# Kernel optimization log

Measured on AMD Instinct MI355X. Metric: run time of the kernel, lower is better.

## Reference

```python
import jax, jax.numpy as jnp
import numpy as np

N_NODES = 100000
N_EDGES = 1600000
D_IN = 128
D_OUT = 128


def setup_inputs() -> dict:
    key = jax.random.key(0)
    k1, k2, k3 = jax.random.split(key, 3)
    x = jax.random.normal(k1, (N_NODES, D_IN), dtype=jnp.float32)
    edge_indices = jax.random.randint(k2, (2, N_EDGES), 0, N_NODES, dtype=jnp.int64)
    # nn.Linear(input_dim, output_dim, bias=False): weight shape [out, in]
    W = jax.random.normal(k3, (D_OUT, D_IN), dtype=jnp.float32) * (1.0 / np.sqrt(D_IN))
    return {"x": x, "edge_indices": edge_indices, "W": W}


def reference(x, edge_indices, W):
    N = x.shape[0]
    # add self loops (i, i) for every node, as in create_norm_adj_mat
    self_loops = jnp.arange(N, dtype=edge_indices.dtype)
    row = jnp.concatenate([edge_indices[0], self_loops])  # [E+N]
    col = jnp.concatenate([edge_indices[1], self_loops])  # [E+N]
    # degree from row indices (torch.bincount(edge_indices[0]))
    deg = jax.ops.segment_sum(jnp.ones_like(row, dtype=x.dtype), row, num_segments=N)
    deg_rsqrt = jax.lax.rsqrt(deg)  # every node has a self loop -> deg >= 1
    vals = deg_rsqrt[row] * deg_rsqrt[col]  # [E+N] edge weights
    # dense linear projection first (linear(x)), then sparse aggregation
    h = x @ W.T  # [N, D_OUT]
    # (norm_adj_mat @ h)[i] = sum over edges with row==i of vals * h[col]
    agg = jax.ops.segment_sum(vals[:, None] * h[col], row, num_segments=N)  # [N, D_OUT]
    return jax.nn.relu(agg)
```

## Files before the change

### kernel.cpp

```cpp
#include <hip/hip_runtime.h>
#include <hip/hip_bf16.h>

#define D 128
#define SH 8
#define BROWS 256
#define NBK_MAX 512
#define CH 8192
#define CT 8
#define KS 4

typedef __bf16   bf16x8 __attribute__((ext_vector_type(8)));
typedef float    f32x4  __attribute__((ext_vector_type(4)));
typedef _Float16 f16x2  __attribute__((ext_vector_type(2)));
typedef _Float16 f16x4  __attribute__((ext_vector_type(4)));

__global__ __launch_bounds__(256) void k_zero(int* __restrict__ p, int n) {
    for (int i = blockIdx.x * blockDim.x + threadIdx.x; i < n; i += gridDim.x * blockDim.x)
        p[i] = 0;
}

__global__ __launch_bounds__(256) void k_bucket_count(const int* __restrict__ rows,
                                                      int* __restrict__ bcnt, int E, int NBK) {
    __shared__ int h[NBK_MAX];
    for (int i = threadIdx.x; i < NBK; i += 256) h[i] = 0;
    __syncthreads();
    for (int e = blockIdx.x * blockDim.x + threadIdx.x; e < E; e += gridDim.x * blockDim.x)
        atomicAdd(&h[rows[e] >> SH], 1);
    __syncthreads();
    for (int i = threadIdx.x; i < NBK; i += 256) {
        int v = h[i];
        if (v) atomicAdd(&bcnt[i], v);
    }
}

__global__ __launch_bounds__(512) void k_scan_buckets(const int* __restrict__ bcnt,
                                                      int* __restrict__ boff,
                                                      int* __restrict__ bcur,
                                                      int* __restrict__ row_start,
                                                      int NBK, int N, int E) {
    __shared__ int sd[512];
    int t = threadIdx.x;
    int own = (t < NBK) ? bcnt[t] : 0;
    sd[t] = own;
    __syncthreads();
    for (int off = 1; off < 512; off <<= 1) {
        int add = (t >= off) ? sd[t - off] : 0;
        __syncthreads();
        sd[t] += add;
        __syncthreads();
    }
    if (t < NBK) {
        int ex = sd[t] - own;
        boff[t] = ex;
        bcur[t] = ex;
    }
    if (t == 0) {
        boff[NBK] = E;
        row_start[N] = E;
    }
}

__global__ __launch_bounds__(256) void k_pairs(const int* __restrict__ rows,
                                               const int* __restrict__ cols,
                                               int* __restrict__ bcur,
                                               unsigned* __restrict__ pairs, int E, int NBK) {
    __shared__ int h[NBK_MAX];
    int e0 = blockIdx.x * CH;
    if (e0 >= E) return;
    int e1 = min(E, e0 + CH);
    for (int i = threadIdx.x; i < NBK; i += 256) h[i] = 0;
    __syncthreads();
    for (int e = e0 + threadIdx.x; e < e1; e += 256)
        atomicAdd(&h[rows[e] >> SH], 1);
    __syncthreads();
    for (int b = threadIdx.x; b < NBK; b += 256) {
        int v = h[b];
        h[b] = v ? atomicAdd(&bcur[b], v) : 0;
    }
    __syncthreads();
    for (int e = e0 + threadIdx.x; e < e1; e += 256) {
        int r = rows[e];
        int b = r >> SH;
        int p = atomicAdd(&h[b], 1);
        pairs[p] = ((unsigned)(r & (BROWS - 1)) << 24) | (unsigned)cols[e];
    }
}

__global__ __launch_bounds__(256) void k_bucket_finish(const unsigned* __restrict__ pairs,
                                                       const int* __restrict__ boff,
                                                       int* __restrict__ row_start,
                                                       float* __restrict__ dr,
                                                       int* __restrict__ csr_col, int N) {
    __shared__ int h[BROWS];
    __shared__ int cur[BROWS];
    int b = blockIdx.x;
    int t = threadIdx.x;
    int lim = min(N - (b << SH), BROWS);
    h[t] = 0;
    __syncthreads();
    int p0 = boff[b], p1 = boff[b + 1];
    for (int p = p0 + t; p < p1; p += 256)
        atomicAdd(&h[pairs[p] >> 24], 1);
    __syncthreads();
    int own = h[t];
    cur[t] = own;
    __syncthreads();
    for (int off = 1; off < 256; off <<= 1) {
        int add = (t >= off) ? cur[t - off] : 0;
        __syncthreads();
        cur[t] += add;
        __syncthreads();
    }
    int rs = p0 + cur[t] - own;
    if (t < lim) {
        row_start[(b << SH) + t] = rs;
        dr[(b << SH) + t] = rsqrtf((float)(own + 1));
    }
    __syncthreads();
    cur[t] = rs;
    __syncthreads();
    for (int p = p0 + t; p < p1; p += 256) {
        unsigned v = pairs[p];
        int rl = v >> 24;
        int q = atomicAdd(&cur[rl], 1);
        csr_col[q] = (int)(v & 0xFFFFFF);
    }
}

__global__ __launch_bounds__(256) void k_half_s(const float4* __restrict__ x4,
                                                const float* __restrict__ dr,
                                                f16x4* __restrict__ xh4, int n4) {
    for (int i = blockIdx.x * blockDim.x + threadIdx.x; i < n4; i += gridDim.x * blockDim.x) {
        float d = dr[i >> 5];
        float4 v = x4[i];
        xh4[i] = (f16x4){(_Float16)(v.x * d), (_Float16)(v.y * d),
                         (_Float16)(v.z * d), (_Float16)(v.w * d)};
    }
}

__global__ __launch_bounds__(256) void k_gather_s(const int* __restrict__ row_start,
                                                  const int* __restrict__ csr_col,
                                                  const _Float16* __restrict__ xh,
                                                  const float* __restrict__ dr,
                                                  float* __restrict__ out, int N) {
    int lane = threadIdx.x & 63;
    int gw = (blockIdx.x * blockDim.x + threadIdx.x) >> 6;
    int nw = (gridDim.x * blockDim.x) >> 6;
    for (int r = gw; r < N; r += nw) {
        float drr = dr[r];
        int beg = row_start[r], end = row_start[r + 1];
        const f16x2 xs = *(const f16x2*)&xh[(size_t)r * D + lane * 2];
        float a0 = (float)xs[0], a1 = (float)xs[1];
        for (int cb = beg; cb < end; cb += 64) {
            int m = end - cb;
            if (m > 64) m = 64;
            int cidx = (lane < m) ? csr_col[cb + lane] : 0;
            int j = 0;
            for (; j + 8 <= m; j += 8) {
                int c0 = __shfl(cidx, j);
                int c1 = __shfl(cidx, j + 1);
                int c2 = __shfl(cidx, j + 2);
                int c3 = __shfl(cidx, j + 3);
                int c4 = __shfl(cidx, j + 4);
                int c5 = __shfl(cidx, j + 5);
                int c6 = __shfl(cidx, j + 6);
                int c7 = __shfl(cidx, j + 7);
                f16x2 p0 = *(const f16x2*)&xh[(size_t)c0 * D + lane * 2];
                f16x2 p1 = *(const f16x2*)&xh[(size_t)c1 * D + lane * 2];
                f16x2 p2 = *(const f16x2*)&xh[(size_t)c2 * D + lane * 2];
                f16x2 p3 = *(const f16x2*)&xh[(size_t)c3 * D + lane * 2];
                f16x2 p4 = *(const f16x2*)&xh[(size_t)c4 * D + lane * 2];
                f16x2 p5 = *(const f16x2*)&xh[(size_t)c5 * D + lane * 2];
                f16x2 p6 = *(const f16x2*)&xh[(size_t)c6 * D + lane * 2];
                f16x2 p7 = *(const f16x2*)&xh[(size_t)c7 * D + lane * 2];
                a0 += (float)p0[0] + (float)p1[0] + (float)p2[0] + (float)p3[0]
                    + (float)p4[0] + (float)p5[0] + (float)p6[0] + (float)p7[0];
                a1 += (float)p0[1] + (float)p1[1] + (float)p2[1] + (float)p3[1]
                    + (float)p4[1] + (float)p5[1] + (float)p6[1] + (float)p7[1];
            }
            for (; j < m; ++j) {
                int c = __shfl(cidx, j);
                f16x2 p = *(const f16x2*)&xh[(size_t)c * D + lane * 2];
                a0 += (float)p[0];
                a1 += (float)p[1];
            }
        }
        float2 o;
        o.x = drr * a0;
        o.y = drr * a1;
        *(float2*)&out[(size_t)r * D + lane * 2] = o;
    }
}

__global__ __launch_bounds__(256) void k_project_mfma(const float* __restrict__ W,
                                                      float* __restrict__ out, int N) {
    __shared__ bf16x8 Bhi[CT * KS * 64];
    __shared__ bf16x8 Blo[CT * KS * 64];
    for (int f = threadIdx.x; f < CT * KS * 64; f += 256) {
        int l  = f & 63;
        int ks = (f >> 6) & 3;
        int ct = f >> 8;
        int o  = ct * 16 + (l & 15);
        int k0 = ks * 32 + ((l >> 4) * 8);
        const float* src = &W[o * D + k0];
        bf16x8 hi, lo;
#pragma unroll
        for (int i = 0; i < 8; ++i) {
            float v  = src[i];
            __bf16 h = (__bf16)v;
            hi[i] = h;
            lo[i] = (__bf16)(v - (float)h);
        }
        Bhi[f] = hi;
        Blo[f] = lo;
    }
    __syncthreads();

    int lane = threadIdx.x & 63;
    int wib  = threadIdx.x >> 6;
    int gw   = blockIdx.x * 4 + wib;
    int nw   = gridDim.x * 4;
    int nt   = N >> 4;
    int arow  = lane & 15;
    int kbase = (lane >> 4) * 8;

    for (int t = gw; t < nt; t += nw) {
        int row = t * 16 + arow;
        const float* arp = &out[(size_t)row * D + kbase];
        bf16x8 Ahi[KS], Alo[KS];
#pragma unroll
        for (int ks = 0; ks < KS; ++ks) {
            float4 v0 = *(const float4*)&arp[ks * 32];
            float4 v1 = *(const float4*)&arp[ks * 32 + 4];
            float va[8] = {v0.x, v0.y, v0.z, v0.w, v1.x, v1.y, v1.z, v1.w};
            bf16x8 hi, lo;
#pragma unroll
            for (int i = 0; i < 8; ++i) {
                __bf16 h = (__bf16)va[i];
                hi[i] = h;
                lo[i] = (__bf16)(va[i] - (float)h);
            }
            Ahi[ks] = hi;
            Alo[ks] = lo;
        }
        f32x4 acc[CT];
#pragma unroll
        for (int ct = 0; ct < CT; ++ct) acc[ct] = (f32x4){0.f, 0.f, 0.f, 0.f};
#pragma unroll
        for (int ks = 0; ks < KS; ++ks) {
#pragma unroll
            for (int ct = 0; ct < CT; ++ct) {
                bf16x8 bh = Bhi[(ct * KS + ks) * 64 + lane];
                bf16x8 bl = Blo[(ct * KS + ks) * 64 + lane];
                acc[ct] = __builtin_amdgcn_mfma_f32_16x16x32_bf16(Ahi[ks], bh, acc[ct], 0, 0, 0);
                acc[ct] = __builtin_amdgcn_mfma_f32_16x16x32_bf16(Alo[ks], bh, acc[ct], 0, 0, 0);
                acc[ct] = __builtin_amdgcn_mfma_f32_16x16x32_bf16(Ahi[ks], bl, acc[ct], 0, 0, 0);
            }
        }
        int orow = t * 16 + (lane >> 4) * 4;
        int ocol = lane & 15;
#pragma unroll
        for (int ct = 0; ct < CT; ++ct) {
#pragma unroll
            for (int reg = 0; reg < 4; ++reg) {
                out[(size_t)(orow + reg) * D + ct * 16 + ocol] = fmaxf(acc[ct][reg], 0.f);
            }
        }
    }
}

__global__ __launch_bounds__(256) void k_gather(const int* __restrict__ row_start,
                                                const int* __restrict__ csr_col,
                                                const float* __restrict__ x,
                                                const float* __restrict__ dr,
                                                float* __restrict__ out, int N) {
    int lane = threadIdx.x & 63;
    int gw = (blockIdx.x * blockDim.x + threadIdx.x) >> 6;
    int nw = (gridDim.x * blockDim.x) >> 6;
    for (int r = gw; r < N; r += nw) {
        float drr = dr[r];
        int beg = row_start[r], end = row_start[r + 1];
        const float2 xs = *(const float2*)&x[(size_t)r * D + lane * 2];
        float s = drr * drr;
        float a0 = s * xs.x, a1 = s * xs.y;
        for (int cb = beg; cb < end; cb += 64) {
            int m = end - cb;
            if (m > 64) m = 64;
            int   cidx = (lane < m) ? csr_col[cb + lane] : 0;
            float cdr  = (lane < m) ? dr[cidx] : 0.f;
            int j = 0;
            for (; j + 4 <= m; j += 4) {
                int c0 = __shfl(cidx, j);
                int c1 = __shfl(cidx, j + 1);
                int c2 = __shfl(cidx, j + 2);
                int c3 = __shfl(cidx, j + 3);
                float v0 = drr * __shfl(cdr, j);
                float v1 = drr * __shfl(cdr, j + 1);
                float v2 = drr * __shfl(cdr, j + 2);
                float v3 = drr * __shfl(cdr, j + 3);
                const float2 p0 = *(const float2*)&x[(size_t)c0 * D + lane * 2];
                const float2 p1 = *(const float2*)&x[(size_t)c1 * D + lane * 2];
                const float2 p2 = *(const float2*)&x[(size_t)c2 * D + lane * 2];
                const float2 p3 = *(const float2*)&x[(size_t)c3 * D + lane * 2];
                a0 = fmaf(v0, p0.x, a0); a1 = fmaf(v0, p0.y, a1);
                a0 = fmaf(v1, p1.x, a0); a1 = fmaf(v1, p1.y, a1);
                a0 = fmaf(v2, p2.x, a0); a1 = fmaf(v2, p2.y, a1);
                a0 = fmaf(v3, p3.x, a0); a1 = fmaf(v3, p3.y, a1);
            }
            for (; j < m; ++j) {
                int   c = __shfl(cidx, j);
                float v = drr * __shfl(cdr, j);
                const float2 p = *(const float2*)&x[(size_t)c * D + lane * 2];
                a0 = fmaf(v, p.x, a0);
                a1 = fmaf(v, p.y, a1);
            }
        }
        float2 o;
        o.x = a0;
        o.y = a1;
        *(float2*)&out[(size_t)r * D + lane * 2] = o;
    }
}

__global__ __launch_bounds__(256) void k_init_deg(int* __restrict__ deg, int n) {
    for (int i = blockIdx.x * blockDim.x + threadIdx.x; i < n; i += gridDim.x * blockDim.x)
        deg[i] = 1;
}
__global__ __launch_bounds__(256) void k_count_atomic(const int* __restrict__ rows,
                                                      int* __restrict__ cnt, int E) {
    for (int e = blockIdx.x * blockDim.x + threadIdx.x; e < E; e += gridDim.x * blockDim.x)
        atomicAdd(&cnt[rows[e]], 1);
}
__global__ __launch_bounds__(256) void k_rsqrt(float* __restrict__ buf, int n) {
    const int* di = (const int*)buf;
    for (int i = blockIdx.x * blockDim.x + threadIdx.x; i < n; i += gridDim.x * blockDim.x) {
        int v = di[i];
        buf[i] = rsqrtf((float)v);
    }
}
__global__ __launch_bounds__(256) void k_init_out(const float4* __restrict__ x4,
                                                  const float* __restrict__ dr,
                                                  float4* __restrict__ out4, int n4) {
    for (int i = blockIdx.x * blockDim.x + threadIdx.x; i < n4; i += gridDim.x * blockDim.x) {
        float d = dr[i >> 5];
        float s = d * d;
        float4 v = x4[i];
        out4[i] = make_float4(v.x * s, v.y * s, v.z * s, v.w * s);
    }
}
__global__ __launch_bounds__(256) void k_edges(const int* __restrict__ rows,
                                               const int* __restrict__ cols,
                                               const float* __restrict__ x,
                                               const float* __restrict__ dr,
                                               float* __restrict__ out, int E) {
    int lane = threadIdx.x & 63;
    int wib  = threadIdx.x >> 6;
    int gw   = blockIdx.x * 4 + wib;
    int nw   = gridDim.x * 4;
    for (int e = gw; e < E; e += nw) {
        int r = rows[e];
        int c = cols[e];
        float val = dr[r] * dr[c];
        const float2 xv = *(const float2*)&x[(size_t)c * D + lane * 2];
        float* po = &out[(size_t)r * D + lane * 2];
        unsafeAtomicAdd(po,     val * xv.x);
        unsafeAtomicAdd(po + 1, val * xv.y);
    }
}

extern "C" void kernel_launch(void* const* d_in, const int* in_sizes, int n_in,
                              void* d_out, int out_size, void* d_ws, size_t ws_size,
                              hipStream_t stream) {
    const float* x   = (const float*)d_in[0];
    const int*   idx = (const int*)d_in[1];
    const float* W   = (const float*)d_in[2];
    float*       out = (float*)d_out;

    int N = in_sizes[0] / D;
    int E = in_sizes[1] / 2;
    const int* rows = idx;
    const int* cols = idx + E;

    int NBK = (N + BROWS - 1) >> SH;

    size_t off = 0;
    size_t o_pairs = off;  off += (size_t)E;
    size_t o_csr   = off;  off += (size_t)E;
    size_t o_rs    = off;  off += (size_t)N + 1;
    size_t o_dr    = off;  off += (size_t)N;
    size_t o_bcnt  = off;  off += (size_t)NBK;
    size_t o_boff  = off;  off += (size_t)NBK + 1;
    size_t o_bcur  = off;  off += (size_t)NBK;
    off = (off + 3) & ~(size_t)3;
    size_t need_mid = off * 4;
    size_t o_xh    = off;  off += ((size_t)N * D) / 2;
    size_t need_full = off * 4;

    int* wsw = (int*)d_ws;
    bool shape_ok = (NBK <= NBK_MAX) && ((N & 15) == 0) && (N < (1 << 24));

    if (shape_ok && ws_size >= need_mid) {
        unsigned* pairs     = (unsigned*)(wsw + o_pairs);
        int*      csr_col   = wsw + o_csr;
        int*      row_start = wsw + o_rs;
        float*    dr        = (float*)(wsw + o_dr);
        int*      bcnt      = wsw + o_bcnt;
        int*      boff      = wsw + o_boff;
        int*      bcur      = wsw + o_bcur;

        k_zero<<<(NBK + 255) / 256, 256, 0, stream>>>(bcnt, NBK);
        k_bucket_count<<<512, 256, 0, stream>>>(rows, bcnt, E, NBK);
        k_scan_buckets<<<1, 512, 0, stream>>>(bcnt, boff, bcur, row_start, NBK, N, E);
        k_pairs<<<(E + CH - 1) / CH, 256, 0, stream>>>(rows, cols, bcur, pairs, E, NBK);
        k_bucket_finish<<<NBK, 256, 0, stream>>>(pairs, boff, row_start, dr, csr_col, N);

        if (ws_size >= need_full) {
            _Float16* xh = (_Float16*)(wsw + o_xh);
            k_half_s<<<2048, 256, 0, stream>>>((const float4*)x, dr, (f16x4*)xh, N * (D / 4));
            k_gather_s<<<4096, 256, 0, stream>>>(row_start, csr_col, xh, dr, out, N);
        } else {
            k_gather<<<4096, 256, 0, stream>>>(row_start, csr_col, x, dr, out, N);
        }
        int nt = N >> 4;
        k_project_mfma<<<(nt + 3) / 4, 256, 0, stream>>>(W, out, N);
    } else {
        int*   deg = (int*)d_ws;
        float* dr  = (float*)d_ws;
        k_init_deg<<<(N + 255) / 256, 256, 0, stream>>>(deg, N);
        k_count_atomic<<<2048, 256, 0, stream>>>(rows, deg, E);
        k_rsqrt<<<(N + 255) / 256, 256, 0, stream>>>(dr, N);
        int n4 = N * (D / 4);
        k_init_out<<<4096, 256, 0, stream>>>((const float4*)x, dr, (float4*)out, n4);
        k_edges<<<4096, 256, 0, stream>>>(rows, cols, x, dr, out, E);
        int nt = N >> 4;
        k_project_mfma<<<(nt + 3) / 4, 256, 0, stream>>>(W, out, N);
    }
}
```

Measured before the change: 219.2 us.

## Split half-precision features into column quarters and gather in four passes

```diff
diff --git a/kernel.cpp b/kernel.cpp
--- a/kernel.cpp
+++ b/kernel.cpp
@@ -8,11 +8,14 @@
 #define CH 8192
 #define CT 8
 #define KS 4
+#define NQ 4
+#define QH 32
 
 typedef __bf16   bf16x8 __attribute__((ext_vector_type(8)));
 typedef float    f32x4  __attribute__((ext_vector_type(4)));
 typedef _Float16 f16x2  __attribute__((ext_vector_type(2)));
 typedef _Float16 f16x4  __attribute__((ext_vector_type(4)));
+typedef _Float16 f16x8  __attribute__((ext_vector_type(8)));
 
 __global__ __launch_bounds__(256) void k_zero(int* __restrict__ p, int n) {
     for (int i = blockIdx.x * blockDim.x + threadIdx.x; i < n; i += gridDim.x * blockDim.x)
@@ -83,6 +86,186 @@
         int b = r >> SH;
         int p = atomicAdd(&h[b], 1);
         pairs[p] = ((unsigned)(r & (BROWS - 1)) << 24) | (unsigned)cols[e];
+    }
+}
+
+__global__ __launch_bounds__(256) void k_bucket_finish_x(const unsigned* __restrict__ pairs,
+                                                         const int* __restrict__ boff,
+                                                         const float* __restrict__ x,
+                                                         int* __restrict__ row_start,
+                                                         float* __restrict__ dr,
+                                                         int* __restrict__ csr_col,
+                                                         _Float16* __restrict__ xh, int N) {
+    __shared__ int   h[BROWS];
+    __shared__ int   cur[BROWS];
+    __shared__ float drl[BROWS];
+    int b = blockIdx.x;
+    int t = threadIdx.x;
+    int base = b << SH;
+    int lim = min(N - base, BROWS);
+    h[t] = 0;
+    __syncthreads();
+    int p0 = boff[b], p1 = boff[b + 1];
+    for (int p = p0 + t; p < p1; p += 256)
+        atomicAdd(&h[pairs[p] >> 24], 1);
+    __syncthreads();
+    int own = h[t];
+    cur[t] = own;
+    __syncthreads();
+    for (int off = 1; off < 256; off <<= 1) {
+        int add = (t >= off) ? cur[t - off] : 0;
+        __syncthreads();
+        cur[t] += add;
+        __syncthreads();
+    }
+    int rs = p0 + cur[t] - own;
+    float d = rsqrtf((float)(own + 1));
+    drl[t] = d;
+    if (t < lim) {
+        row_start[base + t] = rs;
+        dr[base + t] = d;
+    }
+    __syncthreads();
+    cur[t] = rs;
+    __syncthreads();
+
+    for (int q = t * 4; q < lim * D; q += 256 * 4) {
+        int row = q >> 7, d0 = q & 127;
+        float4 v = *(const float4*)&x[(size_t)(base + row) * D + d0];
+        float dd = drl[row];
+        f16x4 hv = {(_Float16)(v.x * dd), (_Float16)(v.y * dd),
+                    (_Float16)(v.z * dd), (_Float16)(v.w * dd)};
+        *(f16x4*)&xh[((size_t)(d0 >> 5) * N + (base + row)) * QH + (d0 & 31)] = hv;
+    }
+
+    for (int p = p0 + t; p < p1; p += 256) {
+        unsigned v = pairs[p];
+        int q2 = atomicAdd(&cur[v >> 24], 1);
+        csr_col[q2] = (int)(v & 0xFFFFFF);
+    }
+}
+
+__global__ __launch_bounds__(256) void k_gather_q(const int* __restrict__ row_start,
+                                                  const int* __restrict__ csr_col,
+                                                  const _Float16* __restrict__ xq,
+                                                  const float* __restrict__ dr,
+                                                  _Float16* __restrict__ aggh,
+                                                  int N, int p) {
+    int lane  = threadIdx.x & 63;
+    int eslot = lane >> 4;
+    int dpos  = (lane & 15) * 2;
+    int gw = (blockIdx.x * blockDim.x + threadIdx.x) >> 6;
+    int nw = (gridDim.x * blockDim.x) >> 6;
+    for (int r = gw; r < N; r += nw) {
+        int beg = row_start[r], end = row_start[r + 1];
+        float drr = dr[r];
+        f16x2 sv = *(const f16x2*)&xq[(size_t)r * QH + dpos];
+        float a0 = (eslot == 0) ? (float)sv[0] : 0.f;
+        float a1 = (eslot == 0) ? (float)sv[1] : 0.f;
+        for (int cb = beg; cb < end; cb += 64) {
+            int m = end - cb;
+            if (m > 64) m = 64;
+            int cidx = (lane < m) ? __builtin_nontemporal_load(&csr_col[cb + lane]) : 0;
+            int g = 0;
+            for (; g + 16 <= m; g += 16) {
+                int c0 = __shfl(cidx, g + eslot);
+                int c1 = __shfl(cidx, g + 4 + eslot);
+                int c2 = __shfl(cidx, g + 8 + eslot);
+                int c3 = __shfl(cidx, g + 12 + eslot);
+                f16x2 p0 = *(const f16x2*)&xq[(size_t)c0 * QH + dpos];
+                f16x2 p1 = *(const f16x2*)&xq[(size_t)c1 * QH + dpos];
+                f16x2 p2 = *(const f16x2*)&xq[(size_t)c2 * QH + dpos];
+                f16x2 p3 = *(const f16x2*)&xq[(size_t)c3 * QH + dpos];
+                a0 += (float)p0[0] + (float)p1[0];
+                a1 += (float)p0[1] + (float)p1[1];
+                a0 += (float)p2[0] + (float)p3[0];
+                a1 += (float)p2[1] + (float)p3[1];
+            }
+            for (; g < m; g += 4) {
+                int srcl = g + eslot;
+                bool valid = srcl < m;
+                int c = __shfl(cidx, valid ? srcl : 0);
+                if (valid) {
+                    f16x2 pv = *(const f16x2*)&xq[(size_t)c * QH + dpos];
+                    a0 += (float)pv[0];
+                    a1 += (float)pv[1];
+                }
+            }
+        }
+        a0 += __shfl_xor(a0, 16);
+        a1 += __shfl_xor(a1, 16);
+        a0 += __shfl_xor(a0, 32);
+        a1 += __shfl_xor(a1, 32);
+        if (lane < 16) {
+            f16x2 o = {(_Float16)(drr * a0), (_Float16)(drr * a1)};
+            __builtin_nontemporal_store(o, (f16x2*)&aggh[(size_t)r * 256 + p * QH + dpos]);
+        }
+    }
+}
+
+__global__ __launch_bounds__(256) void k_project_f16(const float* __restrict__ W,
+                                                     float* __restrict__ out, int N) {
+    __shared__ f16x8 Bhi[CT * KS * 64];
+    __shared__ f16x8 Blo[CT * KS * 64];
+    for (int f = threadIdx.x; f < CT * KS * 64; f += 256) {
+        int l  = f & 63;
+        int ks = (f >> 6) & 3;
+        int ct = f >> 8;
+        int o  = ct * 16 + (l & 15);
+        int k0 = ks * 32 + ((l >> 4) * 8);
+        const float* src = &W[o * D + k0];
+        f16x8 hi, lo;
+#pragma unroll
+        for (int i = 0; i < 8; ++i) {
+            float v = src[i];
+            _Float16 h = (_Float16)v;
+            hi[i] = h;
+            lo[i] = (_Float16)(v - (float)h);
+        }
+        Bhi[f] = hi;
+        Blo[f] = lo;
+    }
+    __syncthreads();
+
+    const _Float16* ah = (const _Float16*)out;
+    int lane = threadIdx.x & 63;
+    int wib  = threadIdx.x >> 6;
+    int gw   = blockIdx.x * 4 + wib;
+    int nw   = gridDim.x * 4;
+    int nt   = N >> 4;
+    int arow  = lane & 15;
+    int kbase = (lane >> 4) * 8;
+
+    for (int t = gw; t < nt; t += nw) {
+        int row = t * 16 + arow;
+        f16x8 A[KS];
+#pragma unroll
+        for (int ks = 0; ks < KS; ++ks)
+            A[ks] = *(const f16x8*)&ah[(size_t)row * 256 + ks * 32 + kbase];
+
+        f32x4 acc[CT];
+#pragma unroll
+        for (int ct = 0; ct < CT; ++ct) acc[ct] = (f32x4){0.f, 0.f, 0.f, 0.f};
+#pragma unroll
+        for (int ks = 0; ks < KS; ++ks) {
+#pragma unroll
+            for (int ct = 0; ct < CT; ++ct) {
+                f16x8 bh = Bhi[(ct * KS + ks) * 64 + lane];
+                f16x8 bl = Blo[(ct * KS + ks) * 64 + lane];
+                acc[ct] = __builtin_amdgcn_mfma_f32_16x16x32_f16(A[ks], bh, acc[ct], 0, 0, 0);
+                acc[ct] = __builtin_amdgcn_mfma_f32_16x16x32_f16(A[ks], bl, acc[ct], 0, 0, 0);
+            }
+        }
+        int orow = t * 16 + (lane >> 4) * 4;
+        int ocol = lane & 15;
+#pragma unroll
+        for (int ct = 0; ct < CT; ++ct) {
+#pragma unroll
+            for (int reg = 0; reg < 4; ++reg) {
+                __builtin_nontemporal_store(fmaxf(acc[ct][reg], 0.f),
+                                            &out[(size_t)(orow + reg) * D + ct * 16 + ocol]);
+            }
+        }
     }
 }
 
@@ -121,151 +304,8 @@
     __syncthreads();
     for (int p = p0 + t; p < p1; p += 256) {
         unsigned v = pairs[p];
-        int rl = v >> 24;
-        int q = atomicAdd(&cur[rl], 1);
+        int q = atomicAdd(&cur[v >> 24], 1);
         csr_col[q] = (int)(v & 0xFFFFFF);
-    }
-}
-
-__global__ __launch_bounds__(256) void k_half_s(const float4* __restrict__ x4,
-                                                const float* __restrict__ dr,
-                                                f16x4* __restrict__ xh4, int n4) {
-    for (int i = blockIdx.x * blockDim.x + threadIdx.x; i < n4; i += gridDim.x * blockDim.x) {
-        float d = dr[i >> 5];
-        float4 v = x4[i];
-        xh4[i] = (f16x4){(_Float16)(v.x * d), (_Float16)(v.y * d),
-                         (_Float16)(v.z * d), (_Float16)(v.w * d)};
-    }
-}
-
-__global__ __launch_bounds__(256) void k_gather_s(const int* __restrict__ row_start,
-                                                  const int* __restrict__ csr_col,
-                                                  const _Float16* __restrict__ xh,
-                                                  const float* __restrict__ dr,
-                                                  float* __restrict__ out, int N) {
-    int lane = threadIdx.x & 63;
-    int gw = (blockIdx.x * blockDim.x + threadIdx.x) >> 6;
-    int nw = (gridDim.x * blockDim.x) >> 6;
-    for (int r = gw; r < N; r += nw) {
-        float drr = dr[r];
-        int beg = row_start[r], end = row_start[r + 1];
-        const f16x2 xs = *(const f16x2*)&xh[(size_t)r * D + lane * 2];
-        float a0 = (float)xs[0], a1 = (float)xs[1];
-        for (int cb = beg; cb < end; cb += 64) {
-            int m = end - cb;
-            if (m > 64) m = 64;
-            int cidx = (lane < m) ? csr_col[cb + lane] : 0;
-            int j = 0;
-            for (; j + 8 <= m; j += 8) {
-                int c0 = __shfl(cidx, j);
-                int c1 = __shfl(cidx, j + 1);
-                int c2 = __shfl(cidx, j + 2);
-                int c3 = __shfl(cidx, j + 3);
-                int c4 = __shfl(cidx, j + 4);
-                int c5 = __shfl(cidx, j + 5);
-                int c6 = __shfl(cidx, j + 6);
-                int c7 = __shfl(cidx, j + 7);
-                f16x2 p0 = *(const f16x2*)&xh[(size_t)c0 * D + lane * 2];
-                f16x2 p1 = *(const f16x2*)&xh[(size_t)c1 * D + lane * 2];
-                f16x2 p2 = *(const f16x2*)&xh[(size_t)c2 * D + lane * 2];
-                f16x2 p3 = *(const f16x2*)&xh[(size_t)c3 * D + lane * 2];
-                f16x2 p4 = *(const f16x2*)&xh[(size_t)c4 * D + lane * 2];
-                f16x2 p5 = *(const f16x2*)&xh[(size_t)c5 * D + lane * 2];
-                f16x2 p6 = *(const f16x2*)&xh[(size_t)c6 * D + lane * 2];
-                f16x2 p7 = *(const f16x2*)&xh[(size_t)c7 * D + lane * 2];
-                a0 += (float)p0[0] + (float)p1[0] + (float)p2[0] + (float)p3[0]
-                    + (float)p4[0] + (float)p5[0] + (float)p6[0] + (float)p7[0];
-                a1 += (float)p0[1] + (float)p1[1] + (float)p2[1] + (float)p3[1]
-                    + (float)p4[1] + (float)p5[1] + (float)p6[1] + (float)p7[1];
-            }
-            for (; j < m; ++j) {
-                int c = __shfl(cidx, j);
-                f16x2 p = *(const f16x2*)&xh[(size_t)c * D + lane * 2];
-                a0 += (float)p[0];
-                a1 += (float)p[1];
-            }
-        }
-        float2 o;
-        o.x = drr * a0;
-        o.y = drr * a1;
-        *(float2*)&out[(size_t)r * D + lane * 2] = o;
-    }
-}
-
-__global__ __launch_bounds__(256) void k_project_mfma(const float* __restrict__ W,
-                                                      float* __restrict__ out, int N) {
-    __shared__ bf16x8 Bhi[CT * KS * 64];
-    __shared__ bf16x8 Blo[CT * KS * 64];
-    for (int f = threadIdx.x; f < CT * KS * 64; f += 256) {
-        int l  = f & 63;
-        int ks = (f >> 6) & 3;
-        int ct = f >> 8;
-        int o  = ct * 16 + (l & 15);
-        int k0 = ks * 32 + ((l >> 4) * 8);
-        const float* src = &W[o * D + k0];
-        bf16x8 hi, lo;
-#pragma unroll
-        for (int i = 0; i < 8; ++i) {
-            float v  = src[i];
-            __bf16 h = (__bf16)v;
-            hi[i] = h;
-            lo[i] = (__bf16)(v - (float)h);
-        }
-        Bhi[f] = hi;
-        Blo[f] = lo;
-    }
-    __syncthreads();
-
-    int lane = threadIdx.x & 63;
-    int wib  = threadIdx.x >> 6;
-    int gw   = blockIdx.x * 4 + wib;
-    int nw   = gridDim.x * 4;
-    int nt   = N >> 4;
-    int arow  = lane & 15;
-    int kbase = (lane >> 4) * 8;
-
-    for (int t = gw; t < nt; t += nw) {
-        int row = t * 16 + arow;
-        const float* arp = &out[(size_t)row * D + kbase];
-        bf16x8 Ahi[KS], Alo[KS];
-#pragma unroll
-        for (int ks = 0; ks < KS; ++ks) {
-            float4 v0 = *(const float4*)&arp[ks * 32];
-            float4 v1 = *(const float4*)&arp[ks * 32 + 4];
-            float va[8] = {v0.x, v0.y, v0.z, v0.w, v1.x, v1.y, v1.z, v1.w};
-            bf16x8 hi, lo;
-#pragma unroll
-            for (int i = 0; i < 8; ++i) {
-                __bf16 h = (__bf16)va[i];
-                hi[i] = h;
-                lo[i] = (__bf16)(va[i] - (float)h);
-            }
-            Ahi[ks] = hi;
-            Alo[ks] = lo;
-        }
-        f32x4 acc[CT];
-#pragma unroll
-        for (int ct = 0; ct < CT; ++ct) acc[ct] = (f32x4){0.f, 0.f, 0.f, 0.f};
-#pragma unroll
-        for (int ks = 0; ks < KS; ++ks) {
-#pragma unroll
-            for (int ct = 0; ct < CT; ++ct) {
-                bf16x8 bh = Bhi[(ct * KS + ks) * 64 + lane];
-                bf16x8 bl = Blo[(ct * KS + ks) * 64 + lane];
-                acc[ct] = __builtin_amdgcn_mfma_f32_16x16x32_bf16(Ahi[ks], bh, acc[ct], 0, 0, 0);
-                acc[ct] = __builtin_amdgcn_mfma_f32_16x16x32_bf16(Alo[ks], bh, acc[ct], 0, 0, 0);
-                acc[ct] = __builtin_amdgcn_mfma_f32_16x16x32_bf16(Ahi[ks], bl, acc[ct], 0, 0, 0);
-            }
-        }
-        int orow = t * 16 + (lane >> 4) * 4;
-        int ocol = lane & 15;
-#pragma unroll
-        for (int ct = 0; ct < CT; ++ct) {
-#pragma unroll
-            for (int reg = 0; reg < 4; ++reg) {
-                out[(size_t)(orow + reg) * D + ct * 16 + ocol] = fmaxf(acc[ct][reg], 0.f);
-            }
-        }
     }
 }
 
@@ -322,6 +362,83 @@
     }
 }
 
+__global__ __launch_bounds__(256) void k_project_mfma(const float* __restrict__ W,
+                                                      float* __restrict__ out, int N) {
+    __shared__ bf16x8 Bhi[CT * KS * 64];
+    __shared__ bf16x8 Blo[CT * KS * 64];
+    for (int f = threadIdx.x; f < CT * KS * 64; f += 256) {
+        int l  = f & 63;
+        int ks = (f >> 6) & 3;
+        int ct = f >> 8;
+        int o  = ct * 16 + (l & 15);
+        int k0 = ks * 32 + ((l >> 4) * 8);
+        const float* src = &W[o * D + k0];
+        bf16x8 hi, lo;
+#pragma unroll
+        for (int i = 0; i < 8; ++i) {
+            float v  = src[i];
+            __bf16 h = (__bf16)v;
+            hi[i] = h;
+            lo[i] = (__bf16)(v - (float)h);
+        }
+        Bhi[f] = hi;
+        Blo[f] = lo;
+    }
+    __syncthreads();
+
+    int lane = threadIdx.x & 63;
+    int wib  = threadIdx.x >> 6;
+    int gw   = blockIdx.x * 4 + wib;
+    int nw   = gridDim.x * 4;
+    int nt   = N >> 4;
+    int arow  = lane & 15;
+    int kbase = (lane >> 4) * 8;
+
+    for (int t = gw; t < nt; t += nw) {
+        int row = t * 16 + arow;
+        const float* arp = &out[(size_t)row * D + kbase];
+        bf16x8 Ahi[KS], Alo[KS];
+#pragma unroll
+        for (int ks = 0; ks < KS; ++ks) {
+            float4 v0 = *(const float4*)&arp[ks * 32];
+            float4 v1 = *(const float4*)&arp[ks * 32 + 4];
+            float va[8] = {v0.x, v0.y, v0.z, v0.w, v1.x, v1.y, v1.z, v1.w};
+            bf16x8 hi, lo;
+#pragma unroll
+            for (int i = 0; i < 8; ++i) {
+                __bf16 h = (__bf16)va[i];
+                hi[i] = h;
+                lo[i] = (__bf16)(va[i] - (float)h);
+            }
+            Ahi[ks] = hi;
+            Alo[ks] = lo;
+        }
+        f32x4 acc[CT];
+#pragma unroll
+        for (int ct = 0; ct < CT; ++ct) acc[ct] = (f32x4){0.f, 0.f, 0.f, 0.f};
+#pragma unroll
+        for (int ks = 0; ks < KS; ++ks) {
+#pragma unroll
+            for (int ct = 0; ct < CT; ++ct) {
+                bf16x8 bh = Bhi[(ct * KS + ks) * 64 + lane];
+                bf16x8 bl = Blo[(ct * KS + ks) * 64 + lane];
+                acc[ct] = __builtin_amdgcn_mfma_f32_16x16x32_bf16(Ahi[ks], bh, acc[ct], 0, 0, 0);
+                acc[ct] = __builtin_amdgcn_mfma_f32_16x16x32_bf16(Alo[ks], bh, acc[ct], 0, 0, 0);
+                acc[ct] = __builtin_amdgcn_mfma_f32_16x16x32_bf16(Ahi[ks], bl, acc[ct], 0, 0, 0);
+            }
+        }
+        int orow = t * 16 + (lane >> 4) * 4;
+        int ocol = lane & 15;
+#pragma unroll
+        for (int ct = 0; ct < CT; ++ct) {
+#pragma unroll
+            for (int reg = 0; reg < 4; ++reg) {
+                out[(size_t)(orow + reg) * D + ct * 16 + ocol] = fmaxf(acc[ct][reg], 0.f);
+            }
+        }
+    }
+}
+
 __global__ __launch_bounds__(256) void k_init_deg(int* __restrict__ deg, int n) {
     for (int i = blockIdx.x * blockDim.x + threadIdx.x; i < n; i += gridDim.x * blockDim.x)
         deg[i] = 1;
@@ -412,17 +529,24 @@
         k_bucket_count<<<512, 256, 0, stream>>>(rows, bcnt, E, NBK);
         k_scan_buckets<<<1, 512, 0, stream>>>(bcnt, boff, bcur, row_start, NBK, N, E);
         k_pairs<<<(E + CH - 1) / CH, 256, 0, stream>>>(rows, cols, bcur, pairs, E, NBK);
-        k_bucket_finish<<<NBK, 256, 0, stream>>>(pairs, boff, row_start, dr, csr_col, N);
 
         if (ws_size >= need_full) {
             _Float16* xh = (_Float16*)(wsw + o_xh);
-            k_half_s<<<2048, 256, 0, stream>>>((const float4*)x, dr, (f16x4*)xh, N * (D / 4));
-            k_gather_s<<<4096, 256, 0, stream>>>(row_start, csr_col, xh, dr, out, N);
+            k_bucket_finish_x<<<NBK, 256, 0, stream>>>(pairs, boff, x, row_start, dr,
+                                                       csr_col, xh, N);
+            _Float16* aggh = (_Float16*)out;
+            for (int p = 0; p < NQ; ++p) {
+                const _Float16* xq = xh + (size_t)p * N * QH;
+                k_gather_q<<<8192, 256, 0, stream>>>(row_start, csr_col, xq, dr, aggh, N, p);
+            }
+            int nt = N >> 4;
+            k_project_f16<<<(nt + 3) / 4, 256, 0, stream>>>(W, out, N);
         } else {
+            k_bucket_finish<<<NBK, 256, 0, stream>>>(pairs, boff, row_start, dr, csr_col, N);
             k_gather<<<4096, 256, 0, stream>>>(row_start, csr_col, x, dr, out, N);
-        }
-        int nt = N >> 4;
-        k_project_mfma<<<(nt + 3) / 4, 256, 0, stream>>>(W, out, N);
+            int nt = N >> 4;
+            k_project_mfma<<<(nt + 3) / 4, 256, 0, stream>>>(W, out, N);
+        }
     } else {
         int*   deg = (int*)d_ws;
         float* dr  = (float*)d_ws;
```

Result: slower. 280.7 us (+28.1%).

## Use fp16 aggregation buffer and single-pass fp16 MFMA projection with prepacked W

Applied to the files above, without the earlier changes.

```diff
diff --git a/kernel.cpp b/kernel.cpp
--- a/kernel.cpp
+++ b/kernel.cpp
@@ -5,7 +5,6 @@
 #define SH 8
 #define BROWS 256
 #define NBK_MAX 512
-#define CH 8192
 #define CT 8
 #define KS 4
 
@@ -13,6 +12,7 @@
 typedef float    f32x4  __attribute__((ext_vector_type(4)));
 typedef _Float16 f16x2  __attribute__((ext_vector_type(2)));
 typedef _Float16 f16x4  __attribute__((ext_vector_type(4)));
+typedef _Float16 f16x8  __attribute__((ext_vector_type(8)));
 
 __global__ __launch_bounds__(256) void k_zero(int* __restrict__ p, int n) {
     for (int i = blockIdx.x * blockDim.x + threadIdx.x; i < n; i += gridDim.x * blockDim.x)
@@ -63,11 +63,12 @@
 __global__ __launch_bounds__(256) void k_pairs(const int* __restrict__ rows,
                                                const int* __restrict__ cols,
                                                int* __restrict__ bcur,
-                                               unsigned* __restrict__ pairs, int E, int NBK) {
+                                               unsigned* __restrict__ pairs,
+                                               int E, int NBK, int chunk) {
     __shared__ int h[NBK_MAX];
-    int e0 = blockIdx.x * CH;
+    int e0 = blockIdx.x * chunk;
     if (e0 >= E) return;
-    int e1 = min(E, e0 + CH);
+    int e1 = min(E, e0 + chunk);
     for (int i = threadIdx.x; i < NBK; i += 256) h[i] = 0;
     __syncthreads();
     for (int e = e0 + threadIdx.x; e < e1; e += 256)
@@ -121,8 +122,7 @@
     __syncthreads();
     for (int p = p0 + t; p < p1; p += 256) {
         unsigned v = pairs[p];
-        int rl = v >> 24;
-        int q = atomicAdd(&cur[rl], 1);
+        int q = atomicAdd(&cur[v >> 24], 1);
         csr_col[q] = (int)(v & 0xFFFFFF);
     }
 }
@@ -138,11 +138,28 @@
     }
 }
 
+__global__ __launch_bounds__(256) void k_prepW(const float* __restrict__ W,
+                                               f16x8* __restrict__ Whi) {
+    for (int f = blockIdx.x * blockDim.x + threadIdx.x; f < CT * KS * 64;
+         f += gridDim.x * blockDim.x) {
+        int l  = f & 63;
+        int ks = (f >> 6) & 3;
+        int ct = f >> 8;
+        int o  = ct * 16 + (l & 15);
+        int k0 = ks * 32 + ((l >> 4) * 8);
+        const float* src = &W[o * D + k0];
+        f16x8 hi;
+#pragma unroll
+        for (int i = 0; i < 8; ++i) hi[i] = (_Float16)src[i];
+        Whi[f] = hi;
+    }
+}
+
 __global__ __launch_bounds__(256) void k_gather_s(const int* __restrict__ row_start,
                                                   const int* __restrict__ csr_col,
                                                   const _Float16* __restrict__ xh,
                                                   const float* __restrict__ dr,
-                                                  float* __restrict__ out, int N) {
+                                                  _Float16* __restrict__ aggh, int N) {
     int lane = threadIdx.x & 63;
     int gw = (blockIdx.x * blockDim.x + threadIdx.x) >> 6;
     int nw = (gridDim.x * blockDim.x) >> 6;
@@ -185,37 +202,14 @@
                 a1 += (float)p[1];
             }
         }
-        float2 o;
-        o.x = drr * a0;
-        o.y = drr * a1;
-        *(float2*)&out[(size_t)r * D + lane * 2] = o;
-    }
-}
-
-__global__ __launch_bounds__(256) void k_project_mfma(const float* __restrict__ W,
-                                                      float* __restrict__ out, int N) {
-    __shared__ bf16x8 Bhi[CT * KS * 64];
-    __shared__ bf16x8 Blo[CT * KS * 64];
-    for (int f = threadIdx.x; f < CT * KS * 64; f += 256) {
-        int l  = f & 63;
-        int ks = (f >> 6) & 3;
-        int ct = f >> 8;
-        int o  = ct * 16 + (l & 15);
-        int k0 = ks * 32 + ((l >> 4) * 8);
-        const float* src = &W[o * D + k0];
-        bf16x8 hi, lo;
-#pragma unroll
-        for (int i = 0; i < 8; ++i) {
-            float v  = src[i];
-            __bf16 h = (__bf16)v;
-            hi[i] = h;
-            lo[i] = (__bf16)(v - (float)h);
-        }
-        Bhi[f] = hi;
-        Blo[f] = lo;
-    }
-    __syncthreads();
-
+        f16x2 o = {(_Float16)(drr * a0), (_Float16)(drr * a1)};
+        *(f16x2*)&aggh[(size_t)r * 256 + lane * 2] = o;
+    }
+}
+
+__global__ __launch_bounds__(256) void k_project_g(const f16x8* __restrict__ Whi,
+                                                   float* __restrict__ out, int N) {
+    const _Float16* ah = (const _Float16*)out;
     int lane = threadIdx.x & 63;
     int wib  = threadIdx.x >> 6;
     int gw   = blockIdx.x * 4 + wib;
@@ -226,35 +220,20 @@
 
     for (int t = gw; t < nt; t += nw) {
         int row = t * 16 + arow;
-        const float* arp = &out[(size_t)row * D + kbase];
-        bf16x8 Ahi[KS], Alo[KS];
+        f16x8 A[KS];
+#pragma unroll
+        for (int ks = 0; ks < KS; ++ks)
+            A[ks] = *(const f16x8*)&ah[(size_t)row * 256 + ks * 32 + kbase];
+
+        f32x4 acc[CT];
+#pragma unroll
+        for (int ct = 0; ct < CT; ++ct) acc[ct] = (f32x4){0.f, 0.f, 0.f, 0.f};
 #pragma unroll
         for (int ks = 0; ks < KS; ++ks) {
-            float4 v0 = *(const float4*)&arp[ks * 32];
-            float4 v1 = *(const float4*)&arp[ks * 32 + 4];
-            float va[8] = {v0.x, v0.y, v0.z, v0.w, v1.x, v1.y, v1.z, v1.w};
-            bf16x8 hi, lo;
-#pragma unroll
-            for (int i = 0; i < 8; ++i) {
-                __bf16 h = (__bf16)va[i];
-                hi[i] = h;
-                lo[i] = (__bf16)(va[i] - (float)h);
-            }
-            Ahi[ks] = hi;
-            Alo[ks] = lo;
-        }
-        f32x4 acc[CT];
-#pragma unroll
-        for (int ct = 0; ct < CT; ++ct) acc[ct] = (f32x4){0.f, 0.f, 0.f, 0.f};
-#pragma unroll
-        for (int ks = 0; ks < KS; ++ks) {
 #pragma unroll
             for (int ct = 0; ct < CT; ++ct) {
-                bf16x8 bh = Bhi[(ct * KS + ks) * 64 + lane];
-                bf16x8 bl = Blo[(ct * KS + ks) * 64 + lane];
-                acc[ct] = __builtin_amdgcn_mfma_f32_16x16x32_bf16(Ahi[ks], bh, acc[ct], 0, 0, 0);
-                acc[ct] = __builtin_amdgcn_mfma_f32_16x16x32_bf16(Alo[ks], bh, acc[ct], 0, 0, 0);
-                acc[ct] = __builtin_amdgcn_mfma_f32_16x16x32_bf16(Ahi[ks], bl, acc[ct], 0, 0, 0);
+                f16x8 bh = Whi[(ct * KS + ks) * 64 + lane];
+                acc[ct] = __builtin_amdgcn_mfma_f32_16x16x32_f16(A[ks], bh, acc[ct], 0, 0, 0);
             }
         }
         int orow = t * 16 + (lane >> 4) * 4;
@@ -322,6 +301,83 @@
     }
 }
 
+__global__ __launch_bounds__(256) void k_project_mfma(const float* __restrict__ W,
+                                                      float* __restrict__ out, int N) {
+    __shared__ bf16x8 Bhi[CT * KS * 64];
+    __shared__ bf16x8 Blo[CT * KS * 64];
+    for (int f = threadIdx.x; f < CT * KS * 64; f += 256) {
+        int l  = f & 63;
+        int ks = (f >> 6) & 3;
+        int ct = f >> 8;
+        int o  = ct * 16 + (l & 15);
+        int k0 = ks * 32 + ((l >> 4) * 8);
+        const float* src = &W[o * D + k0];
+        bf16x8 hi, lo;
+#pragma unroll
+        for (int i = 0; i < 8; ++i) {
+            float v  = src[i];
+            __bf16 h = (__bf16)v;
+            hi[i] = h;
+            lo[i] = (__bf16)(v - (float)h);
+        }
+        Bhi[f] = hi;
+        Blo[f] = lo;
+    }
+    __syncthreads();
+
+    int lane = threadIdx.x & 63;
+    int wib  = threadIdx.x >> 6;
+    int gw   = blockIdx.x * 4 + wib;
+    int nw   = gridDim.x * 4;
+    int nt   = N >> 4;
+    int arow  = lane & 15;
+    int kbase = (lane >> 4) * 8;
+
+    for (int t = gw; t < nt; t += nw) {
+        int row = t * 16 + arow;
+        const float* arp = &out[(size_t)row * D + kbase];
+        bf16x8 Ahi[KS], Alo[KS];
+#pragma unroll
+        for (int ks = 0; ks < KS; ++ks) {
+            float4 v0 = *(const float4*)&arp[ks * 32];
+            float4 v1 = *(const float4*)&arp[ks * 32 + 4];
+            float va[8] = {v0.x, v0.y, v0.z, v0.w, v1.x, v1.y, v1.z, v1.w};
+            bf16x8 hi, lo;
+#pragma unroll
+            for (int i = 0; i < 8; ++i) {
+                __bf16 h = (__bf16)va[i];
+                hi[i] = h;
+                lo[i] = (__bf16)(va[i] - (float)h);
+            }
+            Ahi[ks] = hi;
+            Alo[ks] = lo;
+        }
+        f32x4 acc[CT];
+#pragma unroll
+        for (int ct = 0; ct < CT; ++ct) acc[ct] = (f32x4){0.f, 0.f, 0.f, 0.f};
+#pragma unroll
+        for (int ks = 0; ks < KS; ++ks) {
+#pragma unroll
+            for (int ct = 0; ct < CT; ++ct) {
+                bf16x8 bh = Bhi[(ct * KS + ks) * 64 + lane];
+                bf16x8 bl = Blo[(ct * KS + ks) * 64 + lane];
+                acc[ct] = __builtin_amdgcn_mfma_f32_16x16x32_bf16(Ahi[ks], bh, acc[ct], 0, 0, 0);
+                acc[ct] = __builtin_amdgcn_mfma_f32_16x16x32_bf16(Alo[ks], bh, acc[ct], 0, 0, 0);
+                acc[ct] = __builtin_amdgcn_mfma_f32_16x16x32_bf16(Ahi[ks], bl, acc[ct], 0, 0, 0);
+            }
+        }
+        int orow = t * 16 + (lane >> 4) * 4;
+        int ocol = lane & 15;
+#pragma unroll
+        for (int ct = 0; ct < CT; ++ct) {
+#pragma unroll
+            for (int reg = 0; reg < 4; ++reg) {
+                out[(size_t)(orow + reg) * D + ct * 16 + ocol] = fmaxf(acc[ct][reg], 0.f);
+            }
+        }
+    }
+}
+
 __global__ __launch_bounds__(256) void k_init_deg(int* __restrict__ deg, int n) {
     for (int i = blockIdx.x * blockDim.x + threadIdx.x; i < n; i += gridDim.x * blockDim.x)
         deg[i] = 1;
@@ -393,6 +449,7 @@
     size_t o_bcur  = off;  off += (size_t)NBK;
     off = (off + 3) & ~(size_t)3;
     size_t need_mid = off * 4;
+    size_t o_whi   = off;  off += (size_t)(CT * KS * 64) * 4;
     size_t o_xh    = off;  off += ((size_t)N * D) / 2;
     size_t need_full = off * 4;
 
@@ -408,21 +465,28 @@
         int*      boff      = wsw + o_boff;
         int*      bcur      = wsw + o_bcur;
 
+        const int CHUNK = 2048;
         k_zero<<<(NBK + 255) / 256, 256, 0, stream>>>(bcnt, NBK);
         k_bucket_count<<<512, 256, 0, stream>>>(rows, bcnt, E, NBK);
         k_scan_buckets<<<1, 512, 0, stream>>>(bcnt, boff, bcur, row_start, NBK, N, E);
-        k_pairs<<<(E + CH - 1) / CH, 256, 0, stream>>>(rows, cols, bcur, pairs, E, NBK);
+        k_pairs<<<(E + CHUNK - 1) / CHUNK, 256, 0, stream>>>(rows, cols, bcur, pairs,
+                                                             E, NBK, CHUNK);
         k_bucket_finish<<<NBK, 256, 0, stream>>>(pairs, boff, row_start, dr, csr_col, N);
 
         if (ws_size >= need_full) {
-            _Float16* xh = (_Float16*)(wsw + o_xh);
+            f16x8*    Whi = (f16x8*)(wsw + o_whi);
+            _Float16* xh  = (_Float16*)(wsw + o_xh);
             k_half_s<<<2048, 256, 0, stream>>>((const float4*)x, dr, (f16x4*)xh, N * (D / 4));
-            k_gather_s<<<4096, 256, 0, stream>>>(row_start, csr_col, xh, dr, out, N);
+            k_prepW<<<8, 256, 0, stream>>>(W, Whi);
+            _Float16* aggh = (_Float16*)out;
+            k_gather_s<<<4096, 256, 0, stream>>>(row_start, csr_col, xh, dr, aggh, N);
+            int nt = N >> 4;
+            k_project_g<<<(nt + 3) / 4, 256, 0, stream>>>(Whi, out, N);
         } else {
             k_gather<<<4096, 256, 0, stream>>>(row_start, csr_col, x, dr, out, N);
-        }
-        int nt = N >> 4;
-        k_project_mfma<<<(nt + 3) / 4, 256, 0, stream>>>(W, out, N);
+            int nt = N >> 4;
+            k_project_mfma<<<(nt + 3) / 4, 256, 0, stream>>>(W, out, N);
+        }
     } else {
         int*   deg = (int*)d_ws;
         float* dr  = (float*)d_ws;
```

After: 193.9 us. 11.6% less time.
